# Kernel optimization log

Hardware: AMD Instinct MI355X
Metric: run time of the kernel (lower is better)

The kernel has to match this reference:

```python
import jax, jax.numpy as jnp
import numpy as np

DN = ('NCHW', 'OIHW', 'NCHW')

def conv2d(x, w, b):
    y = jax.lax.conv_general_dilated(x, w, window_strides=(1, 1), padding='SAME', dimension_numbers=DN)
    return y + b[None, :, None, None]

def setup_inputs() -> dict:
    key = jax.random.key(0)
    ks = jax.random.split(key, 8)
    C = 256
    Cq = C // 8
    B, H, W = 8, 56, 56
    fan_out_qk = Cq * 9
    fan_out_v = C * 9
    std_qk = np.sqrt(2.0 / fan_out_qk)  # kaiming_normal fan_out, relu
    std_v = np.sqrt(2.0 / fan_out_v)
    return {
        'x': jax.random.normal(ks[0], (B, C, H, W), dtype=jnp.float32),
        'wq': jax.random.normal(ks[1], (Cq, C, 3, 3), dtype=jnp.float32) * std_qk,
        'bq': jnp.zeros((Cq,), dtype=jnp.float32),
        'wk': jax.random.normal(ks[2], (Cq, C, 3, 3), dtype=jnp.float32) * std_qk,
        'bk': jnp.zeros((Cq,), dtype=jnp.float32),
        'wv': jax.random.normal(ks[3], (C, C, 3, 3), dtype=jnp.float32) * std_v,
        'bv': jnp.zeros((C,), dtype=jnp.float32),
        'gamma': jax.random.uniform(ks[4], (1,), dtype=jnp.float32) * 0.1,
    }

def reference(x, wq, bq, wk, bk, wv, bv, gamma):
    B, C, H, W = x.shape
    N = H * W
    q = conv2d(x, wq, bq).reshape(B, -1, N)   # [B, C/8, N]
    k = conv2d(x, wk, bk).reshape(B, -1, N)   # [B, C/8, N]
    v = conv2d(x, wv, bv).reshape(B, C, N)    # [B, C, N]
    # energy[b,i,j] = sum_d q[b,d,i] * k[b,d,j]  (unscaled)
    energy = jnp.einsum('bdi,bdj->bij', q, k)
    attention = jax.nn.softmax(energy, axis=-1)  # [B, N, N]
    # out[b,c,i] = sum_j v[b,c,j] * attention[b,i,j]
    out = jnp.einsum('bcj,bij->bci', v, attention).reshape(B, C, H, W)
    return gamma[0] * out + x
```

## Files before the change

### kernel.cpp

```cpp
#include <hip/hip_runtime.h>
#include <math.h>

#define B_ 8
#define C_ 256
#define H_ 56
#define W_ 56
#define N_ 3136
#define BN_ (B_*N_)

typedef __attribute__((ext_vector_type(8))) short short8;
typedef __attribute__((ext_vector_type(4))) float f32x4;
typedef __attribute__((ext_vector_type(16))) float f32x16;
typedef __attribute__((ext_vector_type(4))) unsigned short u16x4;
#define MFMA16(A, Bf, Cf) __builtin_amdgcn_mfma_f32_16x16x32_bf16((A), (Bf), (Cf), 0, 0, 0)
#define MFMA32(A, Bf, Cf) __builtin_amdgcn_mfma_f32_32x32x16_bf16((A), (Bf), (Cf), 0, 0, 0)

#define XT_ELEMS (B_*58*64*256)
#define A_ELEMS  (320*2304)
#define AHI_OFF  (2*XT_ELEMS)
#define ALO_OFF  (AHI_OFF + A_ELEMS)
#define QKT_HI_OFF (ALO_OFF + A_ELEMS)
#define QKT_ELEMS  (B_*N_*64)
#define QKT_LO_OFF (QKT_HI_OFF + QKT_ELEMS)
#define VBF_OFF    (QKT_LO_OFF + QKT_ELEMS)
#define VBF_ELEMS  (B_*C_*N_)

#define QF_ELEMS (B_*196*64*8)


#define SWZ(r, col, c8) ((((r)*64 + (col))*4) + ((c8) ^ ((col) & 3)))

#define PSTR 76
#define VSTR 58

__device__ inline unsigned short f2bf(float f) {
    unsigned u = __float_as_uint(f);
    unsigned r = (u + 0x7fffu + ((u >> 16) & 1u)) >> 16;
    return (unsigned short)r;
}
__device__ inline float bf2f(unsigned short h) {
    return __uint_as_float(((unsigned)h) << 16);
}

__global__ __launch_bounds__(256) void zero_pads(uint4* __restrict__ p, int n16)
{
    const int stride = gridDim.x * 256;
    for (int i = blockIdx.x * 256 + threadIdx.x; i < n16; i += stride)
        p[i] = make_uint4(0, 0, 0, 0);
}

__global__ __launch_bounds__(256) void prep_x(
    const float* __restrict__ x,
    unsigned short* __restrict__ xhi, unsigned short* __restrict__ xlo)
{
    __shared__ float xs[64][57];
    const int cc = blockIdx.x, y = blockIdx.y, b = blockIdx.z;
    const int t = threadIdx.x;
    const int c0 = cc * 64;
    for (int idx = t; idx < 64 * 56; idx += 256) {
        const int ch = idx / 56, xc = idx - ch * 56;
        xs[ch][xc] = x[((size_t)(b*C_ + c0 + ch)*H_ + y)*W_ + xc];
    }
    __syncthreads();
    for (int idx = t; idx < 56 * 32; idx += 256) {
        const int xc = idx >> 5, chp = idx & 31;
        const float v0 = xs[2*chp][xc], v1 = xs[2*chp + 1][xc];
        const unsigned short h0 = f2bf(v0), h1 = f2bf(v1);
        const unsigned short l0 = f2bf(v0 - bf2f(h0));
        const unsigned short l1 = f2bf(v1 - bf2f(h1));
        const size_t o = ((size_t)(b*58 + y + 1) * 64 + (xc + 1)) * 256 + c0 + 2*chp;
        *(unsigned*)(xhi + o) = (unsigned)h0 | ((unsigned)h1 << 16);
        *(unsigned*)(xlo + o) = (unsigned)l0 | ((unsigned)l1 << 16);
    }
}

__global__ __launch_bounds__(256) void prep_w(
    const float* __restrict__ wq, const float* __restrict__ wk,
    const float* __restrict__ wv,
    unsigned short* __restrict__ Ahi, unsigned short* __restrict__ Alo)
{
    const int g = blockIdx.x * 256 + threadIdx.x;
    if (g >= 320 * 2304) return;
    const int m = g / 2304, k = g - m * 2304;
    const int s = k >> 8, c = k & 255;
    float w;
    if (m < 32)      w = wq[((size_t)m*C_ + c)*9 + s];
    else if (m < 64) w = wk[((size_t)(m-32)*C_ + c)*9 + s];
    else             w = wv[((size_t)(m-64)*C_ + c)*9 + s];
    const unsigned short h = f2bf(w);
    const int cc = (k >> 5) & 7, quad = (k >> 3) & 3, e = k & 7;
    const size_t o = ((((size_t)(m >> 4)*9 + s)*8 + cc)*64 + (quad*16 + (m & 15)))*8 + e;
    Ahi[o] = h;
    Alo[o] = f2bf(w - bf2f(h));
}

__global__ __launch_bounds__(256) void conv_fused(
    const unsigned short* __restrict__ xhi, const unsigned short* __restrict__ xlo,
    const unsigned short* __restrict__ Ahi, const unsigned short* __restrict__ Alo,
    const float* __restrict__ bq, const float* __restrict__ bk,
    const float* __restrict__ bv,
    unsigned short* __restrict__ qkt_hi, unsigned short* __restrict__ qkt_lo,
    unsigned short* __restrict__ vbf)
{
    __shared__ uint4 SMEM[1552];
    uint4* sH = SMEM;
    uint4* sL = SMEM + 776;
    const int b = blockIdx.x, y = blockIdx.y, z = blockIdx.z;
    const int t = threadIdx.x;
    const int w = t >> 6, L = t & 63;
    const int ln = L & 15, quad = L >> 4;

    if (z == 0) {
        f32x4 acc[4];
#pragma unroll
        for (int nt = 0; nt < 4; nt++) acc[nt] = (f32x4)0.0f;

        uint4 ph[3], pl[3];
#pragma unroll
        for (int i = 0; i < 3; i++) {
            const int idx = t + i*256;
            const int r = idx >> 8, col = (idx >> 2) & 63, c8 = idx & 3;
            const size_t go = ((size_t)((b*58 + y + r)*64 + col))*256 + c8*8;
            ph[i] = *(const uint4*)(xhi + go);
            pl[i] = *(const uint4*)(xlo + go);
        }

        for (int cc = 0; cc < 8; cc++) {
            __syncthreads();
#pragma unroll
            for (int i = 0; i < 3; i++) {
                const int idx = t + i*256;
                const int r = idx >> 8, col = (idx >> 2) & 63, c8 = idx & 3;
                sH[SWZ(r, col, c8)] = ph[i];
                sL[SWZ(r, col, c8)] = pl[i];
            }
            __syncthreads();
            if (cc < 7) {
#pragma unroll
                for (int i = 0; i < 3; i++) {
                    const int idx = t + i*256;
                    const int r = idx >> 8, col = (idx >> 2) & 63, c8 = idx & 3;
                    const size_t go = ((size_t)((b*58 + y + r)*64 + col))*256 + (cc+1)*32 + c8*8;
                    ph[i] = *(const uint4*)(xhi + go);
                    pl[i] = *(const uint4*)(xlo + go);
                }
            }
#pragma unroll
            for (int s = 0; s < 9; s++) {
                const int dx = s % 3 - 1;
                const int r = s / 3;
                const size_t aoff = (((size_t)(w*9 + s)*8 + cc)*64 + L)*8;
                const short8 ah = *(const short8*)(Ahi + aoff);
                const short8 al = *(const short8*)(Alo + aoff);
#pragma unroll
                for (int nt = 0; nt < 4; nt++) {
                    const int col = nt*16 + ln + dx + 1;
                    const int i4 = SWZ(r, col, quad);
                    const short8 bh = *(const short8*)&sH[i4];
                    const short8 bl = *(const short8*)&sL[i4];
                    acc[nt] = MFMA16(ah, bh, acc[nt]);
                    acc[nt] = MFMA16(ah, bl, acc[nt]);
                    acc[nt] = MFMA16(al, bh, acc[nt]);
                }
            }
        }

#pragma unroll
        for (int nt = 0; nt < 4; nt++) {
            const int px = nt*16 + ln;
            if (px >= 56) continue;
            const int pix = y*56 + px;
            u16x4 hi4, lo4;
#pragma unroll
            for (int r = 0; r < 4; r++) {
                const int m = w*16 + quad*4 + r;
                const float bias = (m < 32) ? bq[m] : bk[m - 32];
                const float val = acc[nt][r] + bias;
                const unsigned short h = f2bf(val);
                hi4[r] = h;
                lo4[r] = f2bf(val - bf2f(h));
            }
            const int m0 = w*16 + quad*4;
            size_t o;
            if (w < 2) {
                o = ((size_t)(b*196 + (pix >> 4))*64 + (m0 >> 3)*16 + (pix & 15))*8 + (m0 & 7);
            } else {
                const int mk0 = m0 - 32;
                o = (size_t)QF_ELEMS +
                    (((size_t)(b*49 + (pix >> 6))*4 + ((pix >> 4) & 3))*64
                     + (mk0 >> 3)*16 + (pix & 15))*8 + (mk0 & 7);
            }
            *(u16x4*)(qkt_hi + o) = hi4;
            *(u16x4*)(qkt_lo + o) = lo4;
        }
    } else {
        const int mg = z - 1;

        f32x4 acc[2][4];
#pragma unroll
        for (int g2 = 0; g2 < 2; g2++)
#pragma unroll
            for (int nt = 0; nt < 4; nt++) acc[g2][nt] = (f32x4)0.0f;

        uint4 ph[3];
#pragma unroll
        for (int i = 0; i < 3; i++) {
            const int idx = t + i*256;
            const int r = idx >> 8, col = (idx >> 2) & 63, c8 = idx & 3;
            const size_t go = ((size_t)((b*58 + y + r)*64 + col))*256 + c8*8;
            ph[i] = *(const uint4*)(xhi + go);
        }

        for (int cc = 0; cc < 8; cc++) {
            __syncthreads();
#pragma unroll
            for (int i = 0; i < 3; i++) {
                const int idx = t + i*256;
                const int r = idx >> 8, col = (idx >> 2) & 63, c8 = idx & 3;
                sH[SWZ(r, col, c8)] = ph[i];
            }
            __syncthreads();
            if (cc < 7) {
#pragma unroll
                for (int i = 0; i < 3; i++) {
                    const int idx = t + i*256;
                    const int r = idx >> 8, col = (idx >> 2) & 63, c8 = idx & 3;
                    const size_t go = ((size_t)((b*58 + y + r)*64 + col))*256 + (cc+1)*32 + c8*8;
                    ph[i] = *(const uint4*)(xhi + go);
                }
            }
#pragma unroll
            for (int s = 0; s < 9; s++) {
                const int dx = s % 3 - 1;
                const int r = s / 3;
                const size_t a0off = (((size_t)((4 + mg*8 + w*2)*9 + s)*8 + cc)*64 + L)*8;
                const short8 a0 = *(const short8*)(Ahi + a0off);
                const short8 a1 = *(const short8*)(Ahi + a0off + 9*8*64*8);
#pragma unroll
                for (int nt = 0; nt < 4; nt++) {
                    const int col = nt*16 + ln + dx + 1;
                    const short8 bf = *(const short8*)&sH[SWZ(r, col, quad)];
                    acc[0][nt] = MFMA16(a0, bf, acc[0][nt]);
                    acc[1][nt] = MFMA16(a1, bf, acc[1][nt]);
                }
            }
        }

        __syncthreads();
        unsigned short* Vs = (unsigned short*)SMEM;
#pragma unroll
        for (int g2 = 0; g2 < 2; g2++)
#pragma unroll
            for (int nt = 0; nt < 4; nt++) {
                const int px = nt*16 + ln;
                if (px >= 56) continue;
#pragma unroll
                for (int r = 0; r < 4; r++) {
                    const int cl = (w*2 + g2)*16 + quad*4 + r;
                    Vs[cl*VSTR + px] = f2bf(acc[g2][nt][r] + bv[mg*128 + cl]);
                }
            }
        __syncthreads();
        const int p0 = y*56;
        const int hh = L >> 5, c31 = L & 31;
        const int cg = mg*4 + w;
        const int gend = (p0 + 55) >> 4;
        for (int gi = p0 >> 4; gi <= gend; gi++) {
            const int pxl0 = gi*16 + hh*8 - p0;
            if (pxl0 >= 0 && pxl0 + 8 <= 56) {
                const short8 vv = *(const short8*)&Vs[(w*32 + c31)*VSTR + pxl0];
                const size_t o = ((((size_t)(b*8 + cg)*49 + (gi >> 2))*4 + (gi & 3))*64 + L)*8;
                *(short8*)(vbf + o) = vv;
            }
        }
    }
}

__global__ __launch_bounds__(128, 4) void attn_flash2w(
    const unsigned short* __restrict__ qkt_hi, const unsigned short* __restrict__ qkt_lo,
    const unsigned short* __restrict__ vbf,
    unsigned short* __restrict__ op0, unsigned short* __restrict__ op1,
    float* __restrict__ mlbase)
{
    __shared__ unsigned short P[2][32*PSTR];
    __shared__ float alphaL[2][32];

    const int bx = blockIdx.x;
    const int b = bx & 7, it = bx >> 3;
    const int chalf = blockIdx.y;
    const int jh = blockIdx.z;
    const int jt0 = jh * 25, njt = 25 - jh;
    const int i_base = it * 32;
    const int t = threadIdx.x;
    const int w = t >> 6, L = t & 63;
    const int ln = L & 15, quad = L >> 4;
    const int l32 = L & 31, h32 = L >> 5;

    const unsigned short* Kf_hi = qkt_hi + QF_ELEMS;
    const unsigned short* Kf_lo = qkt_lo + QF_ELEMS;

    const size_t qoff = ((size_t)(b*196 + it*2 + w)*64 + L)*8;
    const short8 qh = *(const short8*)(qkt_hi + qoff);
    const short8 ql = *(const short8*)(qkt_lo + qoff);

    float m_run = -INFINITY, l_run = 0.0f;
    f32x16 O0 = (f32x16)0.0f, O1 = (f32x16)0.0f;
    const int cg0 = chalf*4 + w*2;
    const unsigned short* vt0 = vbf + ((size_t)(b*8 + cg0)*49)*2048 + (size_t)L*8;
    const unsigned short* vt1 = vbf + ((size_t)(b*8 + cg0 + 1)*49)*2048 + (size_t)L*8;
    const unsigned short* kbh = Kf_hi + (size_t)b*49*2048 + (size_t)L*8;
    const unsigned short* kbl = Kf_lo + (size_t)b*49*2048 + (size_t)L*8;

    for (int jtl = 0; jtl < njt; jtl++) {
        const int jt = jt0 + jtl;
        const int buf = jtl & 1;

        short8 Va[4], Vb[4];
#pragma unroll
        for (int s = 0; s < 4; s++) {
            Va[s] = *(const short8*)(vt0 + jt*2048 + s*512);
            Vb[s] = *(const short8*)(vt1 + jt*2048 + s*512);
        }

        f32x4 sacc[4];
#pragma unroll
        for (int tj = 0; tj < 4; tj++) {
            const short8 kh = *(const short8*)(kbh + jt*2048 + tj*512);
            const short8 kl = *(const short8*)(kbl + jt*2048 + tj*512);
            f32x4 a = (f32x4)0.0f;
            a = MFMA16(kh, qh, a);
            a = MFMA16(kh, ql, a);
            a = MFMA16(kl, qh, a);
            sacc[tj] = a;
        }
        float mt0 = fmaxf(fmaxf(sacc[0][0], sacc[0][1]), fmaxf(sacc[0][2], sacc[0][3]));
        float mt1 = fmaxf(fmaxf(sacc[1][0], sacc[1][1]), fmaxf(sacc[1][2], sacc[1][3]));
        float mt2 = fmaxf(fmaxf(sacc[2][0], sacc[2][1]), fmaxf(sacc[2][2], sacc[2][3]));
        float mt3 = fmaxf(fmaxf(sacc[3][0], sacc[3][1]), fmaxf(sacc[3][2], sacc[3][3]));
        float mx = fmaxf(fmaxf(mt0, mt1), fmaxf(mt2, mt3));
        mx = fmaxf(mx, __shfl_xor(mx, 16));
        mx = fmaxf(mx, __shfl_xor(mx, 32));
        const float m_new = fmaxf(m_run, mx);
        const float alpha = __expf(m_run - m_new);
        m_run = m_new;

#pragma unroll
        for (int tj = 0; tj < 4; tj++)
#pragma unroll
            for (int r = 0; r < 4; r++)
                sacc[tj][r] = __expf(sacc[tj][r] - m_new);
        float s0 = (sacc[0][0] + sacc[0][1]) + (sacc[0][2] + sacc[0][3]);
        float s1 = (sacc[1][0] + sacc[1][1]) + (sacc[1][2] + sacc[1][3]);
        float s2 = (sacc[2][0] + sacc[2][1]) + (sacc[2][2] + sacc[2][3]);
        float s3 = (sacc[3][0] + sacc[3][1]) + (sacc[3][2] + sacc[3][3]);
        float ps = (s0 + s1) + (s2 + s3);
        ps += __shfl_xor(ps, 16);
        ps += __shfl_xor(ps, 32);
        l_run = l_run * alpha + ps;

        {
            unsigned short* prow = &P[buf][(w*16 + ln)*PSTR];
#pragma unroll
            for (int tj = 0; tj < 4; tj++) {
                u16x4 pk;
#pragma unroll
                for (int r = 0; r < 4; r++) pk[r] = f2bf(sacc[tj][r]);
                *(u16x4*)(prow + tj*16 + quad*4) = pk;
            }
        }
        if (quad == 0) alphaL[buf][w*16 + ln] = alpha;

        __syncthreads();

        const float a = alphaL[buf][l32];
        if (__any(a != 1.0f)) {
#pragma unroll
            for (int rg = 0; rg < 16; rg++) { O0[rg] *= a; O1[rg] *= a; }
        }
        short8 Bp[4];
#pragma unroll
        for (int s = 0; s < 4; s++) {
            Bp[s] = *(const short8*)&P[buf][l32*PSTR + s*16 + h32*8];
            O0 = MFMA32(Va[s], Bp[s], O0);
        }
#pragma unroll
        for (int s = 0; s < 4; s++)
            O1 = MFMA32(Vb[s], Bp[s], O1);
    }

    if (chalf == 0 && quad == 0) {
        const int i = i_base + w*16 + ln;
        mlbase[jh*BN_ + b*N_ + i]       = m_run;
        mlbase[(2 + jh)*BN_ + b*N_ + i] = l_run;
    }
    unsigned short* OP = jh ? op1 : op0;
    const int pix = i_base + l32;
#pragma unroll
    for (int g = 0; g < 2; g++) {
        const f32x16 Ot = g ? O1 : O0;
        const int cg = chalf*128 + w*64 + g*32;
#pragma unroll
        for (int reg = 0; reg < 16; reg++) {
            const int c = cg + (reg & 3) + 8*(reg >> 2) + 4*h32;
            OP[(size_t)(b*C_ + c)*N_ + pix] = f2bf(Ot[reg]);
        }
    }
}

__global__ __launch_bounds__(256) void combine(
    const unsigned short* __restrict__ op0, const unsigned short* __restrict__ op1,
    const float* __restrict__ mlbase,
    const float* __restrict__ x, const float* __restrict__ gptr,
    float* __restrict__ out)
{
    const int bid = blockIdx.x;
    const int b = bid / 49, pt = bid - b*49;
    const int ch2 = blockIdx.y;
    const int t = threadIdx.x;
    const int pix = pt*64 + (t & 63);
    const int cofs = t >> 6;

    const float m0 = mlbase[b*N_ + pix];
    const float m1 = mlbase[BN_ + b*N_ + pix];
    const float l0 = mlbase[2*BN_ + b*N_ + pix];
    const float l1 = mlbase[3*BN_ + b*N_ + pix];
    const float mm = fmaxf(m0, m1);
    const float a0 = __expf(m0 - mm), a1 = __expf(m1 - mm);
    const float gamma = gptr[0];
    const float inv = gamma / (a0*l0 + a1*l1);
    const float c0 = a0 * inv, c1 = a1 * inv;

    for (int ci = 0; ci < 32; ci++) {
        const int c = ch2*128 + cofs + ci*4;
        const size_t idx = (size_t)(b*C_ + c)*N_ + pix;
        const float o = c0 * bf2f(op0[idx]) + c1 * bf2f(op1[idx]);
        out[idx] = x[idx] + o;
    }
}

extern "C" void kernel_launch(void* const* d_in, const int* in_sizes, int n_in,
                              void* d_out, int out_size, void* d_ws, size_t ws_size,
                              hipStream_t stream)
{
    (void)in_sizes; (void)n_in; (void)out_size; (void)ws_size;
    const float* x  = (const float*)d_in[0];
    const float* wq = (const float*)d_in[1];
    const float* bq = (const float*)d_in[2];
    const float* wk = (const float*)d_in[3];
    const float* bk = (const float*)d_in[4];
    const float* wv = (const float*)d_in[5];
    const float* bv = (const float*)d_in[6];
    const float* gm = (const float*)d_in[7];
    float* out = (float*)d_out;

    unsigned short* u = (unsigned short*)d_ws;
    unsigned short* xhi = u;
    unsigned short* xlo = u + XT_ELEMS;
    unsigned short* Ahi = u + AHI_OFF;
    unsigned short* Alo = u + ALO_OFF;
    unsigned short* qkt_hi = u + QKT_HI_OFF;
    unsigned short* qkt_lo = u + QKT_LO_OFF;
    unsigned short* vbf = u + VBF_OFF;
    float* mlbase = (float*)Ahi;

    hipLaunchKernelGGL(zero_pads, dim3(1024), dim3(256), 0, stream,
                       (uint4*)d_ws, (2*XT_ELEMS*2)/16);
    hipLaunchKernelGGL(prep_x, dim3(4, 56, 8), dim3(256), 0, stream, x, xhi, xlo);
    hipLaunchKernelGGL(prep_w, dim3(2880), dim3(256), 0, stream, wq, wk, wv, Ahi, Alo);
    hipLaunchKernelGGL(conv_fused, dim3(8, 56, 3), dim3(256), 0, stream,
                       xhi, xlo, Ahi, Alo, bq, bk, bv, qkt_hi, qkt_lo, vbf);
    hipLaunchKernelGGL(attn_flash2w, dim3(98*8, 2, 2), dim3(128), 0, stream,
                       qkt_hi, qkt_lo, vbf, xhi, xlo, mlbase);
    hipLaunchKernelGGL(combine, dim3(392, 2), dim3(256), 0, stream,
                       xhi, xlo, mlbase, x, gm, out);
}
```

Measured before the change: 332.7 us.

## Use exp2 softmax with lazy rescale, pad-only zeroing, and vectorized combine

Measured after the change: 324.2 us. 2.6% less time.

```diff
diff --git a/kernel.cpp b/kernel.cpp
--- a/kernel.cpp
+++ b/kernel.cpp
@@ -7,6 +7,7 @@
 #define W_ 56
 #define N_ 3136
 #define BN_ (B_*N_)
+#define LOG2E 1.44269504088896340736f
 
 typedef __attribute__((ext_vector_type(8))) short short8;
 typedef __attribute__((ext_vector_type(4))) float f32x4;
@@ -41,12 +42,29 @@
 __device__ inline float bf2f(unsigned short h) {
     return __uint_as_float(((unsigned)h) << 16);
 }
-
-__global__ __launch_bounds__(256) void zero_pads(uint4* __restrict__ p, int n16)
-{
-    const int stride = gridDim.x * 256;
-    for (int i = blockIdx.x * 256 + threadIdx.x; i < n16; i += stride)
-        p[i] = make_uint4(0, 0, 0, 0);
+__device__ inline float exp2_hw(float x) {
+    float r; asm("v_exp_f32 %0, %1" : "=v"(r) : "v"(x)); return r;
+}
+__device__ inline unsigned cvt_pk_bf16(float lo, float hi) {
+    unsigned r; asm("v_cvt_pk_bf16_f32 %0, %1, %2" : "=v"(r) : "v"(lo), "v"(hi)); return r;
+}
+
+__global__ __launch_bounds__(256) void zero_pads(
+    unsigned short* __restrict__ xhi, unsigned short* __restrict__ xlo)
+{
+    const int g = blockIdx.x*256 + threadIdx.x;
+    const int half = 61440;
+    unsigned short* base = (g < half) ? xhi : xlo;
+    const int i = (g < half) ? g : g - half;
+    const int b = i / 7680, rem = i - b*7680;
+    const int slot = rem >> 5, c8 = rem & 31;
+    int row, col;
+    if (slot < 64)       { row = 0;  col = slot; }
+    else if (slot < 128) { row = 57; col = slot - 64; }
+    else if (slot < 184) { row = slot - 127; col = 0; }
+    else                 { row = slot - 183; col = 57; }
+    const size_t o = ((size_t)((b*58 + row)*64 + col))*256 + c8*8;
+    *(uint4*)(base + o) = make_uint4(0, 0, 0, 0);
 }
 
 __global__ __launch_bounds__(256) void prep_x(
@@ -175,7 +193,8 @@
             for (int r = 0; r < 4; r++) {
                 const int m = w*16 + quad*4 + r;
                 const float bias = (m < 32) ? bq[m] : bk[m - 32];
-                const float val = acc[nt][r] + bias;
+                float val = acc[nt][r] + bias;
+                if (w < 2) val *= LOG2E;
                 const unsigned short h = f2bf(val);
                 hi4[r] = h;
                 lo4[r] = f2bf(val - bf2f(h));
@@ -262,13 +281,13 @@
             }
         __syncthreads();
         const int p0 = y*56;
-        const int hh = L >> 5, c31 = L & 31;
+        const int hh = L >> 5;
         const int cg = mg*4 + w;
         const int gend = (p0 + 55) >> 4;
         for (int gi = p0 >> 4; gi <= gend; gi++) {
             const int pxl0 = gi*16 + hh*8 - p0;
             if (pxl0 >= 0 && pxl0 + 8 <= 56) {
-                const short8 vv = *(const short8*)&Vs[(w*32 + c31)*VSTR + pxl0];
+                const short8 vv = *(const short8*)&Vs[(w*32 + (L & 31))*VSTR + pxl0];
                 const size_t o = ((((size_t)(b*8 + cg)*49 + (gi >> 2))*4 + (gi & 3))*64 + L)*8;
                 *(short8*)(vbf + o) = vv;
             }
@@ -340,15 +359,19 @@
         float mx = fmaxf(fmaxf(mt0, mt1), fmaxf(mt2, mt3));
         mx = fmaxf(mx, __shfl_xor(mx, 16));
         mx = fmaxf(mx, __shfl_xor(mx, 32));
-        const float m_new = fmaxf(m_run, mx);
-        const float alpha = __expf(m_run - m_new);
-        m_run = m_new;
+
+        float alpha = 1.0f;
+        if (__any(mx > m_run + 8.0f)) {
+            const float m_new = fmaxf(m_run, mx);
+            alpha = exp2_hw(m_run - m_new);
+            m_run = m_new;
+        }
 
 #pragma unroll
         for (int tj = 0; tj < 4; tj++)
 #pragma unroll
             for (int r = 0; r < 4; r++)
-                sacc[tj][r] = __expf(sacc[tj][r] - m_new);
+                sacc[tj][r] = exp2_hw(sacc[tj][r] - m_run);
         float s0 = (sacc[0][0] + sacc[0][1]) + (sacc[0][2] + sacc[0][3]);
         float s1 = (sacc[1][0] + sacc[1][1]) + (sacc[1][2] + sacc[1][3]);
         float s2 = (sacc[2][0] + sacc[2][1]) + (sacc[2][2] + sacc[2][3]);
@@ -362,10 +385,10 @@
             unsigned short* prow = &P[buf][(w*16 + ln)*PSTR];
 #pragma unroll
             for (int tj = 0; tj < 4; tj++) {
-                u16x4 pk;
-#pragma unroll
-                for (int r = 0; r < 4; r++) pk[r] = f2bf(sacc[tj][r]);
-                *(u16x4*)(prow + tj*16 + quad*4) = pk;
+                uint2 pp;
+                pp.x = cvt_pk_bf16(sacc[tj][0], sacc[tj][1]);
+                pp.y = cvt_pk_bf16(sacc[tj][2], sacc[tj][3]);
+                *(uint2*)(prow + tj*16 + quad*4) = pp;
             }
         }
         if (quad == 0) alphaL[buf][w*16 + ln] = alpha;
@@ -407,34 +430,52 @@
     }
 }
 
+__global__ __launch_bounds__(256) void coef_pre(
+    const float* __restrict__ mlbase, const float* __restrict__ gptr,
+    float* __restrict__ coef)
+{
+    const int i = blockIdx.x*256 + threadIdx.x;
+    const float m0 = mlbase[i],        m1 = mlbase[BN_ + i];
+    const float l0 = mlbase[2*BN_ + i], l1 = mlbase[3*BN_ + i];
+    const float mm = fmaxf(m0, m1);
+    const float a0 = exp2_hw(m0 - mm), a1 = exp2_hw(m1 - mm);
+    const float inv = gptr[0] / (a0*l0 + a1*l1);
+    coef[2*i]   = a0 * inv;
+    coef[2*i+1] = a1 * inv;
+}
+
 __global__ __launch_bounds__(256) void combine(
     const unsigned short* __restrict__ op0, const unsigned short* __restrict__ op1,
-    const float* __restrict__ mlbase,
-    const float* __restrict__ x, const float* __restrict__ gptr,
-    float* __restrict__ out)
-{
-    const int bid = blockIdx.x;
-    const int b = bid / 49, pt = bid - b*49;
-    const int ch2 = blockIdx.y;
-    const int t = threadIdx.x;
-    const int pix = pt*64 + (t & 63);
-    const int cofs = t >> 6;
-
-    const float m0 = mlbase[b*N_ + pix];
-    const float m1 = mlbase[BN_ + b*N_ + pix];
-    const float l0 = mlbase[2*BN_ + b*N_ + pix];
-    const float l1 = mlbase[3*BN_ + b*N_ + pix];
-    const float mm = fmaxf(m0, m1);
-    const float a0 = __expf(m0 - mm), a1 = __expf(m1 - mm);
-    const float gamma = gptr[0];
-    const float inv = gamma / (a0*l0 + a1*l1);
-    const float c0 = a0 * inv, c1 = a1 * inv;
-
-    for (int ci = 0; ci < 32; ci++) {
-        const int c = ch2*128 + cofs + ci*4;
-        const size_t idx = (size_t)(b*C_ + c)*N_ + pix;
-        const float o = c0 * bf2f(op0[idx]) + c1 * bf2f(op1[idx]);
-        out[idx] = x[idx] + o;
+    const float* __restrict__ coef,
+    const float* __restrict__ x, float* __restrict__ out)
+{
+    const int bc = blockIdx.x;
+    const int b = bc >> 8;
+    const size_t base = (size_t)bc * N_;
+    const float2* cf = (const float2*)coef + (size_t)b * N_;
+    for (int pq = threadIdx.x; pq < 784; pq += 256) {
+        const int p0 = pq * 4;
+        const ushort4 o0 = *(const ushort4*)(op0 + base + p0);
+        const ushort4 o1 = *(const ushort4*)(op1 + base + p0);
+        const float4 xx = *(const float4*)(x + base + p0);
+        float4 r;
+        {
+            const float2 c = cf[p0 + 0];
+            r.x = xx.x + c.x*bf2f(o0.x) + c.y*bf2f(o1.x);
+        }
+        {
+            const float2 c = cf[p0 + 1];
+            r.y = xx.y + c.x*bf2f(o0.y) + c.y*bf2f(o1.y);
+        }
+        {
+            const float2 c = cf[p0 + 2];
+            r.z = xx.z + c.x*bf2f(o0.z) + c.y*bf2f(o1.z);
+        }
+        {
+            const float2 c = cf[p0 + 3];
+            r.w = xx.w + c.x*bf2f(o0.w) + c.y*bf2f(o1.w);
+        }
+        *(float4*)(out + base + p0) = r;
     }
 }
 
@@ -462,15 +503,16 @@
     unsigned short* qkt_lo = u + QKT_LO_OFF;
     unsigned short* vbf = u + VBF_OFF;
     float* mlbase = (float*)Ahi;
-
-    hipLaunchKernelGGL(zero_pads, dim3(1024), dim3(256), 0, stream,
-                       (uint4*)d_ws, (2*XT_ELEMS*2)/16);
+    float* coef = (float*)Alo;
+
+    hipLaunchKernelGGL(zero_pads, dim3(480), dim3(256), 0, stream, xhi, xlo);
     hipLaunchKernelGGL(prep_x, dim3(4, 56, 8), dim3(256), 0, stream, x, xhi, xlo);
     hipLaunchKernelGGL(prep_w, dim3(2880), dim3(256), 0, stream, wq, wk, wv, Ahi, Alo);
     hipLaunchKernelGGL(conv_fused, dim3(8, 56, 3), dim3(256), 0, stream,
                        xhi, xlo, Ahi, Alo, bq, bk, bv, qkt_hi, qkt_lo, vbf);
     hipLaunchKernelGGL(attn_flash2w, dim3(98*8, 2, 2), dim3(128), 0, stream,
                        qkt_hi, qkt_lo, vbf, xhi, xlo, mlbase);
-    hipLaunchKernelGGL(combine, dim3(392, 2), dim3(256), 0, stream,
-                       xhi, xlo, mlbase, x, gm, out);
-}
+    hipLaunchKernelGGL(coef_pre, dim3(98), dim3(256), 0, stream, mlbase, gm, coef);
+    hipLaunchKernelGGL(combine, dim3(2048), dim3(256), 0, stream,
+                       xhi, xlo, coef, x, out);
+}
```
